# Kernel tuning notes

Hardware: AMD Instinct MI355X
Metric: run time of the kernel (lower is better)

The kernel has to match this reference:

```python
import jax, jax.numpy as jnp
import numpy as np

N_HEAD = 8
HID = 64
IN_DIM = 512
OUT_DIM = 512


def setup_inputs() -> dict:
    key = jax.random.key(0)
    ks = jax.random.split(key, 12)
    B, LQ, LK = 2, 2048, 2048
    stdv = 1.0 / np.sqrt(HID)
    inp = {
        "q": jax.random.normal(ks[0], (B, LQ, IN_DIM), jnp.float32),
        "k": jax.random.normal(ks[1], (B, LK, IN_DIM), jnp.float32),
        "v": jax.random.normal(ks[2], (B, LK, IN_DIM), jnp.float32),
        # linear params stored as (in, out); torch Linear applies x @ W.T + b,
        # we store pre-transposed weights so y = x @ W + b is the same math.
        "Wq": jax.random.normal(ks[3], (IN_DIM, N_HEAD * HID), jnp.float32) * 0.02,
        "bq": jnp.zeros((N_HEAD * HID,), jnp.float32),
        "Wk": jax.random.normal(ks[4], (IN_DIM, N_HEAD * HID), jnp.float32) * 0.02,
        "bk": jnp.zeros((N_HEAD * HID,), jnp.float32),
        "Wv": jax.random.normal(ks[5], (IN_DIM, N_HEAD * HID), jnp.float32) * 0.02,
        "bv": jnp.zeros((N_HEAD * HID,), jnp.float32),
        # mlp-method scoring vector, uniform(-stdv, stdv), length 2*hidden
        "w_score": jax.random.uniform(ks[6], (2 * HID,), jnp.float32, -stdv, stdv),
        "Wd": jax.random.normal(ks[7], (N_HEAD * HID, OUT_DIM), jnp.float32) * 0.02,
        "bd": jnp.zeros((OUT_DIM,), jnp.float32),
    }
    return inp


def reference(q, k, v, Wq, bq, Wk, bk, Wv, bv, w_score, Wd, bd):
    B, Lq, _ = q.shape
    Lk = k.shape[1]
    # project and split heads -> (n_head, B, L, hid), matching torch's
    # permute(2,0,1,3).view(n_head*B, L, hid) layout
    qx = (q @ Wq + bq).reshape(B, Lq, N_HEAD, HID).transpose(2, 0, 1, 3)
    kx = (k @ Wk + bk).reshape(B, Lk, N_HEAD, HID).transpose(2, 0, 1, 3)
    vx = (v @ Wv + bv).reshape(B, Lk, N_HEAD, HID).transpose(2, 0, 1, 3)
    # 'mlp' additive attention: tanh(cat(q_i, k_j) . w) == tanh(q_i.w1 + k_j.w2)
    # computed as a broadcast sum instead of materializing the concat tensor
    w1, w2 = w_score[:HID], w_score[HID:]
    qw = qx @ w1  # (n_head, B, Lq)
    kw = kx @ w2  # (n_head, B, Lk)
    score = jnp.tanh(qw[..., :, None] + kw[..., None, :])  # (n_head, B, Lq, Lk)
    score = jax.nn.softmax(score, axis=-1)
    out_head = jnp.einsum('hbqk,hbkd->hbqd', score, vx)  # (n_head, B, Lq, hid)
    # torch: split along head*batch dim then cat along features -> head-major concat
    out = out_head.transpose(1, 2, 0, 3).reshape(B, Lq, N_HEAD * HID)
    output = out @ Wd + bd  # dropout is identity in eval
    score_flat = score.reshape(N_HEAD * B, Lq, Lk)
    return output, score_flat
```

## Files before the change

### kernel.cpp

```cpp
#include <hip/hip_runtime.h>
#include <math.h>

#define B_  2
#define L_  2048
#define D_  512
#define NH_ 8
#define HD_ 64

typedef __attribute__((ext_vector_type(8))) short short8;
typedef __attribute__((ext_vector_type(4))) float f32x4;

__device__ __forceinline__ float ex2(float x) {
#if __has_builtin(__builtin_amdgcn_exp2f)
    return __builtin_amdgcn_exp2f(x);
#else
    return exp2f(x);
#endif
}
__device__ __forceinline__ float rcp_(float x) {
#if __has_builtin(__builtin_amdgcn_rcpf)
    return __builtin_amdgcn_rcpf(x);
#else
    return 1.0f / x;
#endif
}

__device__ __forceinline__ float fast_e(float x) {
    float z  = ex2(x * 2.885390082f);
    float th = 1.0f - 2.0f * rcp_(z + 1.0f);
    return ex2(th * 1.4426950408889634f);
}

__device__ __forceinline__ unsigned int f2bf(float x) {
    unsigned int u = __float_as_uint(x);
    u += 0x7fffu + ((u >> 16) & 1u);
    return u >> 16;
}
__device__ __forceinline__ unsigned int pk2(float lo, float hi) {
    return f2bf(lo) | (f2bf(hi) << 16);
}

__global__ void k_prep(const float* __restrict__ Wq, const float* __restrict__ bq,
                       const float* __restrict__ Wk, const float* __restrict__ bk,
                       const float* __restrict__ wsc,
                       float* __restrict__ wqwT, float* __restrict__ wkwT,
                       float* __restrict__ bqw, float* __restrict__ bkw) {
    __shared__ float w[HD_];
    int which = blockIdx.x >> 1;
    int half  = blockIdx.x & 1;
    const float* W  = which ? Wk : Wq;
    const float* bb = which ? bk : bq;
    float* WT = which ? wkwT : wqwT;
    float* bo = which ? bkw  : bqw;
    if (threadIdx.x < HD_) w[threadIdx.x] = wsc[which * HD_ + threadIdx.x];
    __syncthreads();
    int r = half * 256 + threadIdx.x;
    for (int h = 0; h < NH_; ++h) {
        float s = 0.f;
        #pragma unroll 8
        for (int d = 0; d < HD_; ++d) s += W[r * D_ + h * HD_ + d] * w[d];
        WT[h * D_ + r] = s;
    }
    if (half == 0 && threadIdx.x < NH_) {
        int h = threadIdx.x;
        float s = 0.f;
        for (int d = 0; d < HD_; ++d) s += bb[h * HD_ + d] * w[d];
        bo[h] = s;
    }
}

__global__ void k_wconv(const float* __restrict__ Wv, const float* __restrict__ Wd,
                        unsigned short* __restrict__ WvF,
                        unsigned short* __restrict__ WdFh,
                        unsigned short* __restrict__ WdFl) {
    int id = blockIdx.x * 256 + threadIdx.x;
    int lane = id & 63;
    int kb = (id >> 6) & 15;
    int nf = id >> 10;
    int l15 = lane & 15, lg = lane >> 4;
    int n = nf * 16 + l15;
    int k0 = kb * 32 + lg * 4;
    size_t base = ((size_t)(nf * 16 + kb) * 64 + lane) * 8;
    if (blockIdx.y == 0) {
        #pragma unroll
        for (int j = 0; j < 8; ++j) {
            int k = k0 + (j & 3) + 16 * (j >> 2);
            WvF[base + j] = (unsigned short)f2bf(Wv[(size_t)k * 512 + n]);
        }
    } else {
        #pragma unroll
        for (int j = 0; j < 8; ++j) {
            int k = k0 + (j & 3) + 16 * (j >> 2);
            float x = Wd[(size_t)k * 512 + n];
            unsigned int h = f2bf(x);
            float hf = __uint_as_float(h << 16);
            WdFh[base + j] = (unsigned short)h;
            WdFl[base + j] = (unsigned short)f2bf(x - hf);
        }
    }
}

__global__ void k_qwkw(const float* __restrict__ q, const float* __restrict__ k,
                       const float* __restrict__ wqwT, const float* __restrict__ wkwT,
                       const float* __restrict__ bqw, const float* __restrict__ bkw,
                       float* __restrict__ qw, float* __restrict__ kw) {
    int wid  = blockIdx.x * 4 + (threadIdx.x >> 6);
    int lane = threadIdx.x & 63;
    int sel  = wid >= 4096;
    int row  = wid & 4095;
    const float* src = sel ? k : q;
    const float* WT  = sel ? wkwT : wqwT;
    const float* bo  = sel ? bkw : bqw;
    float* dst = sel ? kw : qw;
    float4 va = *(const float4*)(src + (size_t)row * D_ + lane * 4);
    float4 vb = *(const float4*)(src + (size_t)row * D_ + 256 + lane * 4);
    float res[NH_];
    #pragma unroll
    for (int h = 0; h < NH_; ++h) {
        float4 wa = *(const float4*)(WT + h * D_ + lane * 4);
        float4 wb = *(const float4*)(WT + h * D_ + 256 + lane * 4);
        float s = va.x*wa.x + va.y*wa.y + va.z*wa.z + va.w*wa.w
                + vb.x*wb.x + vb.y*wb.y + vb.z*wb.z + vb.w*wb.w;
        #pragma unroll
        for (int off = 32; off; off >>= 1) s += __shfl_xor(s, off);
        res[h] = s + bo[h];
    }
    if (lane == 0) {
        #pragma unroll
        for (int h = 0; h < NH_; ++h) dst[h * 4096 + row] = res[h];
    }
}

__global__ __launch_bounds__(256) void k_mmA(const float* __restrict__ A,
                                             const short8* __restrict__ BF,
                                             const float* __restrict__ bias,
                                             unsigned short* __restrict__ vxg) {
    int m0 = blockIdx.x * 64;
    int n0q = blockIdx.y * 4;
    int tid = threadIdx.x;
    int w = tid >> 6, lane = tid & 63;
    int l15 = lane & 15, lg = lane >> 4;
    f32x4 acc[4];
    #pragma unroll
    for (int j = 0; j < 4; ++j) acc[j] = (f32x4){0.f, 0.f, 0.f, 0.f};

    const float* a0 = A + (size_t)(m0 + w * 16 + l15) * 512 + lg * 4;

    float4 clo = *(const float4*)(a0);
    float4 chi = *(const float4*)(a0 + 16);
    short8 cb[4];
    #pragma unroll
    for (int nf = 0; nf < 4; ++nf) cb[nf] = BF[(size_t)(n0q + nf) * 16 * 64 + lane];

    for (int kb = 0; kb < 16; ++kb) {
        float4 lo = clo, hi = chi;
        short8 b0 = cb[0], b1 = cb[1], b2 = cb[2], b3 = cb[3];
        if (kb < 15) {
            clo = *(const float4*)(a0 + (kb + 1) * 32);
            chi = *(const float4*)(a0 + (kb + 1) * 32 + 16);
            #pragma unroll
            for (int nf = 0; nf < 4; ++nf)
                cb[nf] = BF[((size_t)(n0q + nf) * 16 + kb + 1) * 64 + lane];
        }
        union { unsigned int u[4]; short8 s; } af;
        af.u[0] = pk2(lo.x, lo.y); af.u[1] = pk2(lo.z, lo.w);
        af.u[2] = pk2(hi.x, hi.y); af.u[3] = pk2(hi.z, hi.w);
        acc[0] = __builtin_amdgcn_mfma_f32_16x16x32_bf16(af.s, b0, acc[0], 0, 0, 0);
        acc[1] = __builtin_amdgcn_mfma_f32_16x16x32_bf16(af.s, b1, acc[1], 0, 0, 0);
        acc[2] = __builtin_amdgcn_mfma_f32_16x16x32_bf16(af.s, b2, acc[2], 0, 0, 0);
        acc[3] = __builtin_amdgcn_mfma_f32_16x16x32_bf16(af.s, b3, acc[3], 0, 0, 0);
    }
    #pragma unroll
    for (int nf = 0; nf < 4; ++nf) {
        int n = (n0q + nf) * 16 + l15;
        float bvv = bias[n];
        int h = n >> 6, dt = (n >> 4) & 3, ncol = n & 15;
        #pragma unroll
        for (int r = 0; r < 4; ++r) {
            int m = m0 + w * 16 + lg * 4 + r;
            int b = m >> 11, kk = m & 2047;
            int kblk = kk >> 5, k32 = kk & 31;
            int lane_v = ncol + 16 * ((k32 >> 2) & 3);
            int ie = (k32 & 3) + 4 * (k32 >> 4);
            size_t ad = ((((size_t)(h * 2 + b) * 64 + kblk) * 4 + dt) * 64 + lane_v) * 8 + ie;
            vxg[ad] = (unsigned short)f2bf(acc[nf][r] + bvv);
        }
    }
}

__global__ __launch_bounds__(256) void k_mmB(const float* __restrict__ A,
                                             const short8* __restrict__ BFh,
                                             const short8* __restrict__ BFl,
                                             const float* __restrict__ bias,
                                             float* __restrict__ C) {
    int m0 = blockIdx.x * 64;
    int n0q = blockIdx.y * 4;
    int tid = threadIdx.x;
    int w = tid >> 6, lane = tid & 63;
    int l15 = lane & 15, lg = lane >> 4;
    f32x4 acc[4];
    #pragma unroll
    for (int j = 0; j < 4; ++j) acc[j] = (f32x4){0.f, 0.f, 0.f, 0.f};

    const float* a0 = A + (size_t)(m0 + w * 16 + l15) * 512 + lg * 4;

    float4 clo = *(const float4*)(a0);
    float4 chi = *(const float4*)(a0 + 16);

    for (int kb = 0; kb < 16; ++kb) {
        float4 lo = clo, hi = chi;
        if (kb < 15) {
            clo = *(const float4*)(a0 + (kb + 1) * 32);
            chi = *(const float4*)(a0 + (kb + 1) * 32 + 16);
        }
        union { unsigned int u[4]; short8 s; } ah, al;
        {
            float xs[8] = {lo.x, lo.y, lo.z, lo.w, hi.x, hi.y, hi.z, hi.w};
            unsigned int hu[8]; float lf[8];
            #pragma unroll
            for (int j = 0; j < 8; ++j) {
                hu[j] = f2bf(xs[j]);
                lf[j] = xs[j] - __uint_as_float(hu[j] << 16);
            }
            #pragma unroll
            for (int j = 0; j < 4; ++j) {
                ah.u[j] = hu[2 * j] | (hu[2 * j + 1] << 16);
                al.u[j] = pk2(lf[2 * j], lf[2 * j + 1]);
            }
        }
        #pragma unroll
        for (int nf = 0; nf < 4; ++nf) {
            size_t bi = ((size_t)(n0q + nf) * 16 + kb) * 64 + lane;
            short8 bh = BFh[bi];
            short8 bl = BFl[bi];
            acc[nf] = __builtin_amdgcn_mfma_f32_16x16x32_bf16(ah.s, bh, acc[nf], 0, 0, 0);
            acc[nf] = __builtin_amdgcn_mfma_f32_16x16x32_bf16(al.s, bh, acc[nf], 0, 0, 0);
            acc[nf] = __builtin_amdgcn_mfma_f32_16x16x32_bf16(ah.s, bl, acc[nf], 0, 0, 0);
        }
    }
    #pragma unroll
    for (int nf = 0; nf < 4; ++nf) {
        int n = (n0q + nf) * 16 + l15;
        float bdv = bias[n];
        #pragma unroll
        for (int r = 0; r < 4; ++r) {
            int m = m0 + w * 16 + lg * 4 + r;
            C[(size_t)m * 512 + n] = acc[nf][r] + bdv;
        }
    }
}

__global__ __launch_bounds__(512, 4) void k_main(const float* __restrict__ qw,
                                                 const float* __restrict__ kw,
                                                 const short8* __restrict__ vgs,
                                                 float* __restrict__ att,
                                                 float* __restrict__ rsum_o) {
    int hb  = blockIdx.y;
    int q0  = blockIdx.x * 64;
    int tid = threadIdx.x;
    int w   = tid >> 6;
    int wq  = w & 3;
    int kh  = w >> 2;
    int lane = tid & 63;
    int l15 = lane & 15, lg = lane >> 4;

    __shared__ float kws[2048];
    __shared__ float red[4][16][68];

    *(float4*)&kws[tid * 4] = *(const float4*)(kw + hb * 2048 + tid * 4);
    __syncthreads();

    float qwv = qw[hb * 2048 + q0 + wq * 16 + l15];
    const short8* bp = vgs + (size_t)hb * 16384 + lane;

    f32x4 acc0 = {0,0,0,0}, acc1 = {0,0,0,0}, acc2 = {0,0,0,0}, acc3 = {0,0,0,0};
    float sum = 0.f;

    int kb0 = kh * 32;
    const short8* pb = bp + (size_t)kb0 * 256;
    short8 cb0 = pb[0], cb1 = pb[64], cb2 = pb[128], cb3 = pb[192];
    float4 ckw0 = *(const float4*)&kws[kb0 * 32 + lg * 4];
    float4 ckw1 = *(const float4*)&kws[kb0 * 32 + lg * 4 + 16];

    for (int i = 0; i < 32; ++i) {
        short8 b0 = cb0, b1 = cb1, b2 = cb2, b3 = cb3;
        float4 kw0 = ckw0, kw1 = ckw1;
        if (i < 31) {
            const short8* nb = bp + (size_t)(kb0 + i + 1) * 256;
            cb0 = nb[0]; cb1 = nb[64]; cb2 = nb[128]; cb3 = nb[192];
            int nk = (kb0 + i + 1) * 32 + lg * 4;
            ckw0 = *(const float4*)&kws[nk];
            ckw1 = *(const float4*)&kws[nk + 16];
        }
        float e0 = fast_e(qwv + kw0.x), e1 = fast_e(qwv + kw0.y);
        float e2 = fast_e(qwv + kw0.z), e3 = fast_e(qwv + kw0.w);
        float e4 = fast_e(qwv + kw1.x), e5 = fast_e(qwv + kw1.y);
        float e6 = fast_e(qwv + kw1.z), e7 = fast_e(qwv + kw1.w);
        sum += ((e0 + e1) + (e2 + e3)) + ((e4 + e5) + (e6 + e7));
        union { unsigned int u[4]; short8 s; } af;
        af.u[0] = pk2(e0, e1);
        af.u[1] = pk2(e2, e3);
        af.u[2] = pk2(e4, e5);
        af.u[3] = pk2(e6, e7);
        acc0 = __builtin_amdgcn_mfma_f32_16x16x32_bf16(af.s, b0, acc0, 0, 0, 0);
        acc1 = __builtin_amdgcn_mfma_f32_16x16x32_bf16(af.s, b1, acc1, 0, 0, 0);
        acc2 = __builtin_amdgcn_mfma_f32_16x16x32_bf16(af.s, b2, acc2, 0, 0, 0);
        acc3 = __builtin_amdgcn_mfma_f32_16x16x32_bf16(af.s, b3, acc3, 0, 0, 0);
    }

    sum += __shfl_xor(sum, 16);
    sum += __shfl_xor(sum, 32);

    if (kh == 1) {
        #define WR_(dt, accv) \
            red[wq][lg * 4 + 0][dt * 16 + l15] = accv[0]; \
            red[wq][lg * 4 + 1][dt * 16 + l15] = accv[1]; \
            red[wq][lg * 4 + 2][dt * 16 + l15] = accv[2]; \
            red[wq][lg * 4 + 3][dt * 16 + l15] = accv[3];
        WR_(0, acc0) WR_(1, acc1) WR_(2, acc2) WR_(3, acc3)
        #undef WR_
        if (lane < 16) red[wq][lane][64] = sum;
    }
    __syncthreads();
    if (kh == 0) {
        #define RD_(dt, accv) \
            accv[0] += red[wq][lg * 4 + 0][dt * 16 + l15]; \
            accv[1] += red[wq][lg * 4 + 1][dt * 16 + l15]; \
            accv[2] += red[wq][lg * 4 + 2][dt * 16 + l15]; \
            accv[3] += red[wq][lg * 4 + 3][dt * 16 + l15];
        RD_(0, acc0) RD_(1, acc1) RD_(2, acc2) RD_(3, acc3)
        #undef RD_
        float tot = sum + red[wq][l15][64];
        float rs = 1.0f / tot;
        if (lane < 16) rsum_o[hb * 2048 + q0 + wq * 16 + lane] = rs;

        int b_ = hb & 1, h = hb >> 1;
        float r0s = __shfl(rs, lg * 4 + 0);
        float r1s = __shfl(rs, lg * 4 + 1);
        float r2s = __shfl(rs, lg * 4 + 2);
        float r3s = __shfl(rs, lg * 4 + 3);
        float* ab = att + ((size_t)(b_ * 2048 + q0 + wq * 16 + lg * 4)) * 512 + h * 64 + l15;
        #define ST_(dt, accv) \
            ab[0 * 512 + dt * 16] = accv[0] * r0s; \
            ab[1 * 512 + dt * 16] = accv[1] * r1s; \
            ab[2 * 512 + dt * 16] = accv[2] * r2s; \
            ab[3 * 512 + dt * 16] = accv[3] * r3s;
        ST_(0, acc0) ST_(1, acc1) ST_(2, acc2) ST_(3, acc3)
        #undef ST_
    }
}

__global__ void k_score(const float* __restrict__ qw, const float* __restrict__ kw,
                        const float* __restrict__ rsum, float* __restrict__ score) {
    int hb = blockIdx.y;
    int tid = threadIdx.x;
    __shared__ float kws[2048];
    *(float4*)&kws[tid * 8]     = *(const float4*)(kw + hb * 2048 + tid * 8);
    *(float4*)&kws[tid * 8 + 4] = *(const float4*)(kw + hb * 2048 + tid * 8 + 4);
    __syncthreads();
    int rl  = tid >> 5;
    int t32 = tid & 31;
    int q = blockIdx.x * 8 + rl;
    float qwv = qw[hb * 2048 + q];
    float rs  = rsum[hb * 2048 + q];
    float* out = score + ((size_t)(hb * 2048 + q)) * 2048;
    #pragma unroll
    for (int i = 0; i < 16; ++i) {
        int k = i * 128 + t32 * 4;
        float4 o;
        o.x = fast_e(qwv + kws[k + 0]) * rs;
        o.y = fast_e(qwv + kws[k + 1]) * rs;
        o.z = fast_e(qwv + kws[k + 2]) * rs;
        o.w = fast_e(qwv + kws[k + 3]) * rs;
        *(float4*)(out + k) = o;
    }
}

extern "C" void kernel_launch(void* const* d_in, const int* in_sizes, int n_in,
                              void* d_out, int out_size, void* d_ws, size_t ws_size,
                              hipStream_t stream) {
    (void)in_sizes; (void)n_in; (void)out_size; (void)ws_size;
    const float* q   = (const float*)d_in[0];
    const float* k   = (const float*)d_in[1];
    const float* v   = (const float*)d_in[2];
    const float* Wq  = (const float*)d_in[3];
    const float* bq  = (const float*)d_in[4];
    const float* Wk  = (const float*)d_in[5];
    const float* bk  = (const float*)d_in[6];
    const float* Wv  = (const float*)d_in[7];
    const float* bv  = (const float*)d_in[8];
    const float* wsc = (const float*)d_in[9];
    const float* Wd  = (const float*)d_in[10];
    const float* bd  = (const float*)d_in[11];

    float* out   = (float*)d_out;
    float* score = out + (size_t)B_ * L_ * D_;

    float* ws    = (float*)d_ws;
    float* wqwT  = ws;
    float* wkwT  = ws + 4096;
    float* bqw   = ws + 8192;
    float* bkw   = ws + 8256;
    float* qw    = ws + 8704;
    float* kw    = ws + 41472;
    float* rsum  = ws + 74240;
    float* vxg   = ws + 107008;
    float* att   = ws + 1155584;
    float* WvF   = ws + 3252736;
    float* WdFh  = ws + 3383808;
    float* WdFl  = ws + 3514880;

    k_prep<<<dim3(4), dim3(256), 0, stream>>>(Wq, bq, Wk, bk, wsc, wqwT, wkwT, bqw, bkw);
    k_wconv<<<dim3(128, 2), dim3(256), 0, stream>>>(Wv, Wd,
        (unsigned short*)WvF, (unsigned short*)WdFh, (unsigned short*)WdFl);
    k_qwkw<<<dim3(2048), dim3(256), 0, stream>>>(q, k, wqwT, wkwT, bqw, bkw, qw, kw);
    k_mmA<<<dim3(64, 8), dim3(256), 0, stream>>>(v, (const short8*)WvF, bv,
        (unsigned short*)vxg);
    k_main<<<dim3(32, 16), dim3(512), 0, stream>>>(qw, kw, (const short8*)vxg, att, rsum);
    k_score<<<dim3(256, 16), dim3(256), 0, stream>>>(qw, kw, rsum, score);
    k_mmB<<<dim3(64, 8), dim3(256), 0, stream>>>(att, (const short8*)WdFh,
        (const short8*)WdFl, bd, out);
}
```

Before: 164.1 us.

## Precompute softmax row sums and fuse score writes into attention kernel

Adds a small kernel that computes each row's softmax denominator up front. The main attention kernel then normalizes the probabilities before the MFMA and writes the score matrix directly, which removes the separate score kernel. The exp work is now done twice (rsum pass plus main) instead of twice before (main plus score), but one full launch and a second pass over the data go away. In exchange, the 128MB score write now sits inside the MFMA loop with a strided per-row store pattern, which could slow the main kernel.

Result: no change. 165.5 us (+0.8%).

```diff
diff --git a/kernel.cpp b/kernel.cpp
--- a/kernel.cpp
+++ b/kernel.cpp
@@ -131,6 +131,27 @@
     }
 }
 
+__global__ __launch_bounds__(256) void k_rsum(const float* __restrict__ qw,
+                                              const float* __restrict__ kw,
+                                              float* __restrict__ rsum) {
+    int hb   = blockIdx.y;
+    int widx = threadIdx.x >> 6;
+    int lane = threadIdx.x & 63;
+    int r = blockIdx.x * 4 + widx;
+    float qwv = qw[hb * 2048 + r];
+    const float* kp = kw + hb * 2048;
+    float s = 0.f;
+    #pragma unroll
+    for (int j = 0; j < 8; ++j) {
+        float4 v = *(const float4*)(kp + j * 256 + lane * 4);
+        s += (fast_e(qwv + v.x) + fast_e(qwv + v.y))
+           + (fast_e(qwv + v.z) + fast_e(qwv + v.w));
+    }
+    #pragma unroll
+    for (int off = 32; off; off >>= 1) s += __shfl_xor(s, off);
+    if (lane == 0) rsum[hb * 2048 + r] = 1.0f / s;
+}
+
 __global__ __launch_bounds__(256) void k_mmA(const float* __restrict__ A,
                                              const short8* __restrict__ BF,
                                              const float* __restrict__ bias,
@@ -253,8 +274,9 @@
 __global__ __launch_bounds__(512, 4) void k_main(const float* __restrict__ qw,
                                                  const float* __restrict__ kw,
                                                  const short8* __restrict__ vgs,
+                                                 const float* __restrict__ rsum,
                                                  float* __restrict__ att,
-                                                 float* __restrict__ rsum_o) {
+                                                 float* __restrict__ score) {
     int hb  = blockIdx.y;
     int q0  = blockIdx.x * 64;
     int tid = threadIdx.x;
@@ -270,17 +292,20 @@
     *(float4*)&kws[tid * 4] = *(const float4*)(kw + hb * 2048 + tid * 4);
     __syncthreads();
 
-    float qwv = qw[hb * 2048 + q0 + wq * 16 + l15];
+    int qrow = q0 + wq * 16 + l15;
+    float qwv = qw[hb * 2048 + qrow];
+    float rs  = rsum[hb * 2048 + qrow];
     const short8* bp = vgs + (size_t)hb * 16384 + lane;
 
     f32x4 acc0 = {0,0,0,0}, acc1 = {0,0,0,0}, acc2 = {0,0,0,0}, acc3 = {0,0,0,0};
-    float sum = 0.f;
 
     int kb0 = kh * 32;
     const short8* pb = bp + (size_t)kb0 * 256;
     short8 cb0 = pb[0], cb1 = pb[64], cb2 = pb[128], cb3 = pb[192];
     float4 ckw0 = *(const float4*)&kws[kb0 * 32 + lg * 4];
     float4 ckw1 = *(const float4*)&kws[kb0 * 32 + lg * 4 + 16];
+
+    float* sp = score + ((size_t)(hb * 2048 + qrow)) * 2048 + kb0 * 32 + lg * 4;
 
     for (int i = 0; i < 32; ++i) {
         short8 b0 = cb0, b1 = cb1, b2 = cb2, b3 = cb3;
@@ -292,11 +317,10 @@
             ckw0 = *(const float4*)&kws[nk];
             ckw1 = *(const float4*)&kws[nk + 16];
         }
-        float e0 = fast_e(qwv + kw0.x), e1 = fast_e(qwv + kw0.y);
-        float e2 = fast_e(qwv + kw0.z), e3 = fast_e(qwv + kw0.w);
-        float e4 = fast_e(qwv + kw1.x), e5 = fast_e(qwv + kw1.y);
-        float e6 = fast_e(qwv + kw1.z), e7 = fast_e(qwv + kw1.w);
-        sum += ((e0 + e1) + (e2 + e3)) + ((e4 + e5) + (e6 + e7));
+        float e0 = fast_e(qwv + kw0.x) * rs, e1 = fast_e(qwv + kw0.y) * rs;
+        float e2 = fast_e(qwv + kw0.z) * rs, e3 = fast_e(qwv + kw0.w) * rs;
+        float e4 = fast_e(qwv + kw1.x) * rs, e5 = fast_e(qwv + kw1.y) * rs;
+        float e6 = fast_e(qwv + kw1.z) * rs, e7 = fast_e(qwv + kw1.w) * rs;
         union { unsigned int u[4]; short8 s; } af;
         af.u[0] = pk2(e0, e1);
         af.u[1] = pk2(e2, e3);
@@ -306,10 +330,11 @@
         acc1 = __builtin_amdgcn_mfma_f32_16x16x32_bf16(af.s, b1, acc1, 0, 0, 0);
         acc2 = __builtin_amdgcn_mfma_f32_16x16x32_bf16(af.s, b2, acc2, 0, 0, 0);
         acc3 = __builtin_amdgcn_mfma_f32_16x16x32_bf16(af.s, b3, acc3, 0, 0, 0);
-    }
-
-    sum += __shfl_xor(sum, 16);
-    sum += __shfl_xor(sum, 32);
+        float4 s0 = {e0, e1, e2, e3};
+        float4 s1 = {e4, e5, e6, e7};
+        *(float4*)(sp + i * 32)      = s0;
+        *(float4*)(sp + i * 32 + 16) = s1;
+    }
 
     if (kh == 1) {
         #define WR_(dt, accv) \
@@ -319,60 +344,18 @@
             red[wq][lg * 4 + 3][dt * 16 + l15] = accv[3];
         WR_(0, acc0) WR_(1, acc1) WR_(2, acc2) WR_(3, acc3)
         #undef WR_
-        if (lane < 16) red[wq][lane][64] = sum;
     }
     __syncthreads();
     if (kh == 0) {
-        #define RD_(dt, accv) \
-            accv[0] += red[wq][lg * 4 + 0][dt * 16 + l15]; \
-            accv[1] += red[wq][lg * 4 + 1][dt * 16 + l15]; \
-            accv[2] += red[wq][lg * 4 + 2][dt * 16 + l15]; \
-            accv[3] += red[wq][lg * 4 + 3][dt * 16 + l15];
-        RD_(0, acc0) RD_(1, acc1) RD_(2, acc2) RD_(3, acc3)
-        #undef RD_
-        float tot = sum + red[wq][l15][64];
-        float rs = 1.0f / tot;
-        if (lane < 16) rsum_o[hb * 2048 + q0 + wq * 16 + lane] = rs;
-
         int b_ = hb & 1, h = hb >> 1;
-        float r0s = __shfl(rs, lg * 4 + 0);
-        float r1s = __shfl(rs, lg * 4 + 1);
-        float r2s = __shfl(rs, lg * 4 + 2);
-        float r3s = __shfl(rs, lg * 4 + 3);
         float* ab = att + ((size_t)(b_ * 2048 + q0 + wq * 16 + lg * 4)) * 512 + h * 64 + l15;
         #define ST_(dt, accv) \
-            ab[0 * 512 + dt * 16] = accv[0] * r0s; \
-            ab[1 * 512 + dt * 16] = accv[1] * r1s; \
-            ab[2 * 512 + dt * 16] = accv[2] * r2s; \
-            ab[3 * 512 + dt * 16] = accv[3] * r3s;
+            ab[0 * 512 + dt * 16] = accv[0] + red[wq][lg * 4 + 0][dt * 16 + l15]; \
+            ab[1 * 512 + dt * 16] = accv[1] + red[wq][lg * 4 + 1][dt * 16 + l15]; \
+            ab[2 * 512 + dt * 16] = accv[2] + red[wq][lg * 4 + 2][dt * 16 + l15]; \
+            ab[3 * 512 + dt * 16] = accv[3] + red[wq][lg * 4 + 3][dt * 16 + l15];
         ST_(0, acc0) ST_(1, acc1) ST_(2, acc2) ST_(3, acc3)
         #undef ST_
-    }
-}
-
-__global__ void k_score(const float* __restrict__ qw, const float* __restrict__ kw,
-                        const float* __restrict__ rsum, float* __restrict__ score) {
-    int hb = blockIdx.y;
-    int tid = threadIdx.x;
-    __shared__ float kws[2048];
-    *(float4*)&kws[tid * 8]     = *(const float4*)(kw + hb * 2048 + tid * 8);
-    *(float4*)&kws[tid * 8 + 4] = *(const float4*)(kw + hb * 2048 + tid * 8 + 4);
-    __syncthreads();
-    int rl  = tid >> 5;
-    int t32 = tid & 31;
-    int q = blockIdx.x * 8 + rl;
-    float qwv = qw[hb * 2048 + q];
-    float rs  = rsum[hb * 2048 + q];
-    float* out = score + ((size_t)(hb * 2048 + q)) * 2048;
-    #pragma unroll
-    for (int i = 0; i < 16; ++i) {
-        int k = i * 128 + t32 * 4;
-        float4 o;
-        o.x = fast_e(qwv + kws[k + 0]) * rs;
-        o.y = fast_e(qwv + kws[k + 1]) * rs;
-        o.z = fast_e(qwv + kws[k + 2]) * rs;
-        o.w = fast_e(qwv + kws[k + 3]) * rs;
-        *(float4*)(out + k) = o;
     }
 }
 
@@ -414,10 +397,11 @@
     k_wconv<<<dim3(128, 2), dim3(256), 0, stream>>>(Wv, Wd,
         (unsigned short*)WvF, (unsigned short*)WdFh, (unsigned short*)WdFl);
     k_qwkw<<<dim3(2048), dim3(256), 0, stream>>>(q, k, wqwT, wkwT, bqw, bkw, qw, kw);
+    k_rsum<<<dim3(512, 16), dim3(256), 0, stream>>>(qw, kw, rsum);
     k_mmA<<<dim3(64, 8), dim3(256), 0, stream>>>(v, (const short8*)WvF, bv,
         (unsigned short*)vxg);
-    k_main<<<dim3(32, 16), dim3(512), 0, stream>>>(qw, kw, (const short8*)vxg, att, rsum);
-    k_score<<<dim3(256, 16), dim3(256), 0, stream>>>(qw, kw, rsum, score);
+    k_main<<<dim3(32, 16), dim3(512), 0, stream>>>(qw, kw, (const short8*)vxg,
+        rsum, att, score);
     k_mmB<<<dim3(64, 8), dim3(256), 0, stream>>>(att, (const short8*)WdFh,
         (const short8*)WdFl, bd, out);
 }
```
